# Performance work log

Hardware: AMD Instinct MI355X
Metric: run time of the kernel (lower is better)

## Reference

```python
import jax, jax.numpy as jnp
import numpy as np

NQ = 4            # num_qubits
NL = 2            # num_layer
NA = NL * (4 * NQ - 1)  # 30 angles total


def _apply_1q(state, U, w):
    # state: (B, 2,2,2,2) complex64; U: (B, 2, 2); wire w (qubit 0 = axis 1)
    s = jnp.moveaxis(state, 1 + w, -1)
    sh = s.shape
    s = s.reshape(sh[0], -1, 2)
    s = jnp.einsum('bij,bkj->bki', U, s)
    return jnp.moveaxis(s.reshape(sh), -1, 1 + w)


def _apply_2q(state, U, w):
    # two-qubit gate on wires (w, w+1); U: (B, 4, 4)
    s = jnp.moveaxis(state, (1 + w, 2 + w), (-2, -1))
    sh = s.shape
    s = s.reshape(sh[0], -1, 4)
    s = jnp.einsum('bij,bkj->bki', U, s)
    return jnp.moveaxis(s.reshape(sh), (-2, -1), (1 + w, 2 + w))


def _u3(theta, phi, lam):
    # U3(theta, phi, lam) = [[cos(t/2), -e^{il} sin(t/2)], [e^{ip} sin(t/2), e^{i(p+l)} cos(t/2)]]
    c = jnp.cos(theta / 2).astype(jnp.complex64)
    s = jnp.sin(theta / 2).astype(jnp.complex64)
    el = jnp.exp(1j * lam.astype(jnp.complex64))
    ep = jnp.exp(1j * phi.astype(jnp.complex64))
    row0 = jnp.stack([c, -el * s], axis=-1)
    row1 = jnp.stack([ep * s, ep * el * c], axis=-1)
    return jnp.stack([row0, row1], axis=-2)  # (B, 2, 2)


def _rxx(theta):
    # exp(-i theta/2 XX)
    c = jnp.cos(theta / 2).astype(jnp.complex64)
    ms = (-1j) * jnp.sin(theta / 2).astype(jnp.complex64)
    z = jnp.zeros_like(c)
    rows = [[c, z, z, ms], [z, c, ms, z], [z, ms, c, z], [ms, z, z, c]]
    return jnp.stack([jnp.stack(r, axis=-1) for r in rows], axis=-2)  # (B, 4, 4)


def _circuit(angles):
    # angles: (B, 30) float; returns (B, 16) complex64 statevector, init |0000>
    B = angles.shape[0]
    psi = jnp.zeros((B, 2 ** NQ), jnp.complex64).at[:, 0].set(1.0)
    psi = psi.reshape((B,) + (2,) * NQ)
    per_layer = 4 * NQ - 1
    for lay in range(NL):
        a = angles[:, lay * per_layer:(lay + 1) * per_layer]
        k = 0
        for i in range(NQ - 1):
            psi = _apply_2q(psi, _rxx(a[:, k]), i)
            k += 1
            psi = _apply_1q(psi, _u3(a[:, k], a[:, k + 1], a[:, k + 2]), i)
            k += 3
        psi = _apply_1q(psi, _u3(a[:, k], a[:, k + 1], a[:, k + 2]), NQ - 1)
    return psi.reshape(B, 2 ** NQ)


def setup_inputs() -> dict:
    key = jax.random.key(0)
    k1, k2, k3 = jax.random.split(key, 3)
    B, D = 65536, 784
    return {
        'input': jax.random.normal(k1, (B, D), dtype=jnp.float32),
        'W': jax.random.normal(k2, (NA, D), dtype=jnp.float32) * 0.05,
        'b': jax.random.normal(k3, (NA,), dtype=jnp.float32) * 0.05,
    }


def reference(input, W, b):
    angles = input @ W.T + b            # Linear(input_size -> num_angles)
    psi = _circuit(angles)              # (B, 16) complex statevector in qdev
    # return as float [B, 16, 2] = (real, imag)
    return jnp.stack([psi.real, psi.imag], axis=-1)
```

## Files before the change

kernel.cpp:

```cpp
#include <hip/hip_runtime.h>
#include <math.h>

constexpr int KDIM  = 784;
constexpr int NA    = 30;
constexpr int KC    = 32;
constexpr int ROWS  = 64;
constexpr int NW    = 4;
constexpr int NT    = NW * 64;
constexpr int APT   = 8;
constexpr int NCH   = 24;
constexpr int KTAIL = 16;

__global__ __launch_bounds__(NT, 4)
void fused_rnn_circuit(const float* __restrict__ X,
                       const float* __restrict__ W,
                       const float* __restrict__ Bv,
                       float* __restrict__ out)
{
    const int t    = threadIdx.x;
    const int lane = t & 63;
    const int w    = t >> 6;
    const long long row0 = (long long)blockIdx.x * ROWS;

    __shared__ float xs[2][ROWS * KC];
    __shared__ float ang[ROWS][33];

    const int srow = t >> 3;
    const int sq   = (t & 7) ^ (srow & 7);
    const float* gsrc0 = X + (row0 + srow)      * (long long)KDIM + sq * 4;
    const float* gsrc1 = X + (row0 + 32 + srow) * (long long)KDIM + sq * 4;

    auto stage = [&](int c, int buf) {
        const float* g0 = gsrc0 + c * KC;
        const float* g1 = gsrc1 + c * KC;
        __builtin_amdgcn_global_load_lds(
            (const __attribute__((address_space(1))) void*)g0,
            (__attribute__((address_space(3))) void*)&xs[buf][w * 256], 16, 0, 0);
        __builtin_amdgcn_global_load_lds(
            (const __attribute__((address_space(1))) void*)g1,
            (__attribute__((address_space(3))) void*)&xs[buf][1024 + w * 256], 16, 0, 0);
    };

    const int r  = lane;
    const int rx = r & 7;
    int arj[APT];
#pragma unroll
    for (int j = 0; j < APT; ++j) {
        int a = w * APT + j;
        arj[j] = __builtin_amdgcn_readfirstlane(a < NA ? a : NA - 1);
    }

    float acc[APT];
#pragma unroll
    for (int j = 0; j < APT; ++j) acc[j] = 0.f;

    stage(0, 0);
    __syncthreads();

    for (int c = 0; c < NCH; ++c) {
        const int buf = c & 1;
        if (c + 1 < NCH) stage(c + 1, buf ^ 1);

        float xv[KC];
#pragma unroll
        for (int q = 0; q < 8; ++q) {
            float4 v = *reinterpret_cast<const float4*>(&xs[buf][r * KC + ((q ^ rx) << 2)]);
            xv[4 * q + 0] = v.x; xv[4 * q + 1] = v.y;
            xv[4 * q + 2] = v.z; xv[4 * q + 3] = v.w;
        }

#pragma unroll
        for (int j = 0; j < APT; ++j) {
            const float* wr = W + (long long)arj[j] * KDIM + c * KC;
            float s = acc[j];
#pragma unroll
            for (int k = 0; k < KC; ++k) s = fmaf(xv[k], wr[k], s);
            acc[j] = s;
        }
        __syncthreads();
    }

    {
        const float* xt = X + (row0 + r) * (long long)KDIM + NCH * KC;
        float xv[KTAIL];
#pragma unroll
        for (int q = 0; q < 4; ++q) {
            float4 v = *reinterpret_cast<const float4*>(xt + 4 * q);
            xv[4 * q + 0] = v.x; xv[4 * q + 1] = v.y;
            xv[4 * q + 2] = v.z; xv[4 * q + 3] = v.w;
        }
#pragma unroll
        for (int j = 0; j < APT; ++j) {
            const float* wr = W + (long long)arj[j] * KDIM + NCH * KC;
            float s = acc[j];
#pragma unroll
            for (int k = 0; k < KTAIL; ++k) s = fmaf(xv[k], wr[k], s);
            acc[j] = s;
        }
    }

#pragma unroll
    for (int j = 0; j < APT; ++j) {
        int a = w * APT + j;
        if (a < NA) ang[r][a] = acc[j] + Bv[a];
    }
    __syncthreads();

    if (t < 64) {
        const float* ap = ang[t];

        float sr[16], si[16];
#pragma unroll
        for (int q = 0; q < 16; ++q) { sr[q] = 0.f; si[q] = 0.f; }
        sr[0] = 1.f;

        auto u3 = [&](int wq, float th, float ph, float la) {
            float ch, sh;  __sincosf(0.5f * th, &sh, &ch);
            float elr, eli; __sincosf(la, &eli, &elr);
            float epr, epi; __sincosf(ph, &epi, &epr);
            float eer = epr * elr - epi * eli;
            float eei = epr * eli + epi * elr;
            const int m = 1 << (3 - wq);
#pragma unroll
            for (int idx = 0; idx < 16; ++idx) {
                if (idx & m) continue;
                int i1 = idx + m;
                float o0r = sr[idx], o0i = si[idx], o1r = sr[i1], o1i = si[i1];
                float e1r = elr * o1r - eli * o1i;
                float e1i = elr * o1i + eli * o1r;
                sr[idx] = ch * o0r - sh * e1r;
                si[idx] = ch * o0i - sh * e1i;
                float p0r = epr * o0r - epi * o0i;
                float p0i = epr * o0i + epi * o0r;
                float q1r = eer * o1r - eei * o1i;
                float q1i = eer * o1i + eei * o1r;
                sr[i1] = sh * p0r + ch * q1r;
                si[i1] = sh * p0i + ch * q1i;
            }
        };

#pragma unroll
        for (int lay = 0; lay < 2; ++lay) {
            const int base = lay * 15;
#pragma unroll
            for (int i = 0; i < 3; ++i) {
                {
                    float th = ap[base + i * 4];
                    float ch, sh; __sincosf(0.5f * th, &sh, &ch);
                    const int m1 = 1 << (3 - i);
                    const int m2 = 1 << (2 - i);
#pragma unroll
                    for (int b0 = 0; b0 < 16; ++b0) {
                        if (b0 & (m1 | m2)) continue;
                        int i00 = b0, i01 = b0 + m2, i10 = b0 + m1, i11 = b0 + m1 + m2;
                        float o00r = sr[i00], o00i = si[i00], o11r = sr[i11], o11i = si[i11];
                        sr[i00] = ch * o00r + sh * o11i;
                        si[i00] = ch * o00i - sh * o11r;
                        sr[i11] = ch * o11r + sh * o00i;
                        si[i11] = ch * o11i - sh * o00r;
                        float o01r = sr[i01], o01i = si[i01], o10r = sr[i10], o10i = si[i10];
                        sr[i01] = ch * o01r + sh * o10i;
                        si[i01] = ch * o01i - sh * o10r;
                        sr[i10] = ch * o10r + sh * o01i;
                        si[i10] = ch * o10i - sh * o01r;
                    }
                }
                u3(i, ap[base + i * 4 + 1], ap[base + i * 4 + 2], ap[base + i * 4 + 3]);
            }
            u3(3, ap[base + 12], ap[base + 13], ap[base + 14]);
        }

        float* orow = out + (row0 + t) * 32;
#pragma unroll
        for (int q = 0; q < 8; ++q) {
            float4 v = make_float4(sr[2 * q], si[2 * q], sr[2 * q + 1], si[2 * q + 1]);
            *reinterpret_cast<float4*>(orow + q * 4) = v;
        }
    }
}

extern "C" void kernel_launch(void* const* d_in, const int* in_sizes, int n_in,
                              void* d_out, int out_size, void* d_ws, size_t ws_size,
                              hipStream_t stream) {
    const float* X  = (const float*)d_in[0];
    const float* W  = (const float*)d_in[1];
    const float* Bv = (const float*)d_in[2];
    float* out = (float*)d_out;

    const int Bn = in_sizes[0] / KDIM;
    dim3 grid(Bn / ROWS);
    fused_rnn_circuit<<<grid, NT, 0, stream>>>(X, W, Bv, out);
}
```

Measured before the change: 103.1 us.

## Triple-buffer X staging with explicit vmcnt waits and prefetch tail to LDS

Replaces the double-buffered K-chunk loop with a manually unrolled three-buffer pipeline. It waits on `s_waitcnt vmcnt(2)` plus a raw `s_barrier` instead of `__syncthreads`, so two chunk loads stay in flight while the current chunk is computed. The 16-element K tail is now fetched asynchronously into LDS at the start instead of read directly from global memory at the end. The angle buffer is aliased onto the staging buffers, and the min-blocks launch bound is dropped. In exchange, LDS use per block goes up, and correctness now depends on the hand-counted vmcnt values and on the aliasing order.

```diff
diff --git a/kernel.cpp b/kernel.cpp
--- a/kernel.cpp
+++ b/kernel.cpp
@@ -6,12 +6,15 @@
 constexpr int KC    = 32;
 constexpr int ROWS  = 64;
 constexpr int NW    = 4;
-constexpr int NT    = NW * 64;
+constexpr int NT    = 256;
 constexpr int APT   = 8;
 constexpr int NCH   = 24;
 constexpr int KTAIL = 16;
 
-__global__ __launch_bounds__(NT, 4)
+#define WAIT_VM(N) asm volatile("s_waitcnt vmcnt(" #N ")" ::: "memory")
+#define BARRIER()  do { __builtin_amdgcn_s_barrier(); asm volatile("" ::: "memory"); } while (0)
+
+__global__ __launch_bounds__(NT)
 void fused_rnn_circuit(const float* __restrict__ X,
                        const float* __restrict__ W,
                        const float* __restrict__ Bv,
@@ -22,8 +25,8 @@
     const int w    = t >> 6;
     const long long row0 = (long long)blockIdx.x * ROWS;
 
-    __shared__ float xs[2][ROWS * KC];
-    __shared__ float ang[ROWS][33];
+    __shared__ float xs[3][ROWS * KC];
+    __shared__ float xst[ROWS * 16];
 
     const int srow = t >> 3;
     const int sq   = (t & 7) ^ (srow & 7);
@@ -31,13 +34,11 @@
     const float* gsrc1 = X + (row0 + 32 + srow) * (long long)KDIM + sq * 4;
 
     auto stage = [&](int c, int buf) {
-        const float* g0 = gsrc0 + c * KC;
-        const float* g1 = gsrc1 + c * KC;
         __builtin_amdgcn_global_load_lds(
-            (const __attribute__((address_space(1))) void*)g0,
+            (const __attribute__((address_space(1))) void*)(gsrc0 + c * KC),
             (__attribute__((address_space(3))) void*)&xs[buf][w * 256], 16, 0, 0);
         __builtin_amdgcn_global_load_lds(
-            (const __attribute__((address_space(1))) void*)g1,
+            (const __attribute__((address_space(1))) void*)(gsrc1 + c * KC),
             (__attribute__((address_space(3))) void*)&xs[buf][1024 + w * 256], 16, 0, 0);
     };
 
@@ -54,13 +55,7 @@
 #pragma unroll
     for (int j = 0; j < APT; ++j) acc[j] = 0.f;
 
-    stage(0, 0);
-    __syncthreads();
-
-    for (int c = 0; c < NCH; ++c) {
-        const int buf = c & 1;
-        if (c + 1 < NCH) stage(c + 1, buf ^ 1);
-
+    auto compute = [&](int j, int buf) {
         float xv[KC];
 #pragma unroll
         for (int q = 0; q < 8; ++q) {
@@ -68,37 +63,55 @@
             xv[4 * q + 0] = v.x; xv[4 * q + 1] = v.y;
             xv[4 * q + 2] = v.z; xv[4 * q + 3] = v.w;
         }
-
-#pragma unroll
-        for (int j = 0; j < APT; ++j) {
-            const float* wr = W + (long long)arj[j] * KDIM + c * KC;
-            float s = acc[j];
+#pragma unroll
+        for (int a = 0; a < APT; ++a) {
+            const float* wr = W + (long long)arj[a] * KDIM + j * KC;
+            float s = acc[a];
 #pragma unroll
             for (int k = 0; k < KC; ++k) s = fmaf(xv[k], wr[k], s);
-            acc[j] = s;
-        }
-        __syncthreads();
-    }
-
+            acc[a] = s;
+        }
+    };
+
+    stage(0, 0);
+    stage(1, 1);
     {
-        const float* xt = X + (row0 + r) * (long long)KDIM + NCH * KC;
+        const float* gp = X + (row0 + (t >> 2)) * (long long)KDIM + NCH * KC + (t & 3) * 4;
+        __builtin_amdgcn_global_load_lds(
+            (const __attribute__((address_space(1))) void*)gp,
+            (__attribute__((address_space(3))) void*)&xst[w * 256], 16, 0, 0);
+    }
+    WAIT_VM(3);
+    BARRIER();
+
+    for (int jj = 0; jj < 21; jj += 3) {
+        stage(jj + 2, 2); compute(jj + 0, 0); WAIT_VM(2); BARRIER();
+        stage(jj + 3, 0); compute(jj + 1, 1); WAIT_VM(2); BARRIER();
+        stage(jj + 4, 1); compute(jj + 2, 2); WAIT_VM(2); BARRIER();
+    }
+    stage(23, 2); compute(21, 0); WAIT_VM(2); BARRIER();
+    compute(22, 1);               WAIT_VM(0); BARRIER();
+    compute(23, 2);
+
+    {
         float xv[KTAIL];
 #pragma unroll
         for (int q = 0; q < 4; ++q) {
-            float4 v = *reinterpret_cast<const float4*>(xt + 4 * q);
+            float4 v = *reinterpret_cast<const float4*>(&xst[r * 16 + 4 * q]);
             xv[4 * q + 0] = v.x; xv[4 * q + 1] = v.y;
             xv[4 * q + 2] = v.z; xv[4 * q + 3] = v.w;
         }
 #pragma unroll
-        for (int j = 0; j < APT; ++j) {
-            const float* wr = W + (long long)arj[j] * KDIM + NCH * KC;
-            float s = acc[j];
+        for (int a = 0; a < APT; ++a) {
+            const float* wr = W + (long long)arj[a] * KDIM + NCH * KC;
+            float s = acc[a];
 #pragma unroll
             for (int k = 0; k < KTAIL; ++k) s = fmaf(xv[k], wr[k], s);
-            acc[j] = s;
-        }
-    }
-
+            acc[a] = s;
+        }
+    }
+
+    float (*ang)[33] = reinterpret_cast<float (*)[33]>(&xs[0][0]);
 #pragma unroll
     for (int j = 0; j < APT; ++j) {
         int a = w * APT + j;
```

Measured after the change: 230.2 us. +123.3%, slower.
